# Performance work log

Hardware: AMD Instinct MI355X
Metric: run time of the kernel (lower is better)

## Reference

```python
import jax, jax.numpy as jnp
import numpy as np

N = 64          # truth table size (2^6)
NUM_VARS = 6
TOP_K = 16
BATCH = 524288
IN_DIM = 17 + TOP_K  # 33
HID = 64
OUT = 64
EPS_LN = 1e-5


def _hadamard(n: int) -> np.ndarray:
    H = np.array([[1.0]], dtype=np.float32)
    while H.shape[0] < n:
        H = np.block([[H, H], [H, -H]])
    return H

_HAMMING = np.array([bin(i).count('1') for i in range(N)], dtype=np.float32)


def _xavier(key, fan_in, fan_out):
    lim = np.sqrt(6.0 / (fan_in + fan_out)).astype(np.float32)
    return jax.random.uniform(key, (fan_in, fan_out), jnp.float32, -lim, lim)


def setup_inputs() -> dict:
    key = jax.random.key(0)
    ks = jax.random.split(key, 4)
    truth_table = jax.random.randint(ks[0], (BATCH, N), 0, 2).astype(jnp.int32)
    H = jnp.asarray(_hadamard(N))
    return {
        'truth_table': truth_table,
        'H': H,
        'W1': _xavier(ks[1], IN_DIM, HID), 'b1': jnp.zeros((HID,), jnp.float32),
        'g1': jnp.ones((HID,), jnp.float32), 'be1': jnp.zeros((HID,), jnp.float32),
        'W2': _xavier(ks[2], HID, HID), 'b2': jnp.zeros((HID,), jnp.float32),
        'g2': jnp.ones((HID,), jnp.float32), 'be2': jnp.zeros((HID,), jnp.float32),
        'W3': _xavier(ks[3], HID, OUT), 'b3': jnp.zeros((OUT,), jnp.float32),
    }


def _layernorm(x, g, b):
    m = jnp.mean(x, axis=-1, keepdims=True)
    v = jnp.mean((x - m) ** 2, axis=-1, keepdims=True)
    return (x - m) / jnp.sqrt(v + EPS_LN) * g + b


def _walsh_features(truth_table, H):
    # Walsh-Hadamard transform: torch.mm(H, f.T).T == f @ H.T == f @ H (H symmetric)
    f_polar = 1.0 - 2.0 * truth_table.astype(jnp.float32)  # [B, 64]
    walsh = f_polar @ H                                     # [B, 64]
    walsh_abs = jnp.abs(walsh)
    walsh_sq = walsh * walsh
    n = jnp.float32(N)

    # --- key coefficients (8d): W(0), W(2^i) i=0..5, W(n-1) ---
    key_idx = jnp.array([0, 1, 2, 4, 8, 16, 32, N - 1])
    key_coeffs = walsh[:, key_idx] / n                      # [B, 8]

    # --- spectral statistics (5d) ---
    threshold = 0.1 * n
    sparsity = jnp.mean((walsh_abs < threshold).astype(jnp.float32), axis=1, keepdims=True)
    max_abs = jnp.max(walsh_abs, axis=1, keepdims=True)
    max_mag = max_abs / n
    l1 = jnp.sum(walsh_abs, axis=1, keepdims=True) / (n * n)
    sumsq = jnp.sum(walsh_sq, axis=1, keepdims=True)
    l2 = jnp.sqrt(sumsq) / (n * n)
    p = walsh_sq / (sumsq + 1e-10)
    entropy = -jnp.sum(p * jnp.log(p + 1e-10), axis=1, keepdims=True) / jnp.log(n)
    spectral = jnp.concatenate([sparsity, max_mag, l1, l2, entropy], axis=1)  # [B, 5]

    # --- linearity indicators (4d) ---
    large_coeffs = jnp.sum((walsh_abs > 0.5 * n).astype(jnp.float32), axis=1, keepdims=True)
    is_linear = ((large_coeffs >= 1) & (large_coeffs <= 2)).astype(jnp.float32)
    nonlinearity = jnp.clip(0.5 - max_abs / (2 * n), 0.0, 0.5) * 2.0
    hw = jnp.asarray(_HAMMING)
    large_mask = (walsh_abs > threshold).astype(jnp.float32)
    degree = jnp.sum(large_mask * hw, axis=1, keepdims=True) / (
        jnp.sum(large_mask, axis=1, keepdims=True) + 1e-10) / NUM_VARS
    bent_mag = jnp.float32(2.0 ** (NUM_VARS / 2))  # 8.0
    bent_dev = jnp.mean(jnp.abs(walsh_abs - bent_mag) / bent_mag, axis=1, keepdims=True)
    is_bent = (bent_dev < 0.1).astype(jnp.float32)
    linearity = jnp.concatenate([is_linear, nonlinearity, degree, is_bent], axis=1)  # [B, 4]

    # --- top-k |W| coefficients (16d) ---
    topk = jax.lax.top_k(walsh_abs, TOP_K)[0] / n            # [B, 16]

    return jnp.concatenate([key_coeffs, spectral, linearity, topk], axis=1)  # [B, 33]


def reference(truth_table, H, W1, b1, g1, be1, W2, b2, g2, be2, W3, b3):
    feats = _walsh_features(truth_table, H)
    h = jax.nn.gelu(_layernorm(feats @ W1 + b1, g1, be1), approximate=False)
    # Dropout(0.1) is identity in eval mode
    h = jax.nn.gelu(_layernorm(h @ W2 + b2, g2, be2), approximate=False)
    return h @ W3 + b3  # [B, 64]
```

## Files before the change

kernel.cpp:

```cpp
#include <hip/hip_runtime.h>
#include <math.h>

#define TPB 256

typedef _Float16 half8 __attribute__((ext_vector_type(8)));
typedef _Float16 h2 __attribute__((ext_vector_type(2)));
typedef float f32x4 __attribute__((ext_vector_type(4)));

__device__ __forceinline__ int swz(int row, int col) {
    return row * 64 + ((((col >> 3) ^ row) & 7) << 3) + (col & 7);
}

__device__ __forceinline__ unsigned int pk_f16(float a, float b) {
    auto p = __builtin_amdgcn_cvt_pkrtz(a, b);
    return __builtin_bit_cast(unsigned int, p);
}

__device__ __forceinline__ float gelu_sig(float x) {
    float u = x * fmaf(0.0713548162f, x * x, 1.595769122f);
    float e = __expf(-u);
    return x * __builtin_amdgcn_rcpf(1.0f + e);
}

__device__ __forceinline__ void ce2(h2& x, h2& y) {
    h2 mx = __builtin_elementwise_max(x, y);
    h2 mn = __builtin_elementwise_min(x, y);
    x = mx; y = mn;
}

template<int CTRL>
__device__ __forceinline__ f32x4 dpp_add4(f32x4 x) {
#pragma unroll
    for (int r = 0; r < 4; ++r) {
        int o = __builtin_amdgcn_update_dpp(0, __float_as_int(x[r]),
                                            CTRL, 0xf, 0xf, false);
        x[r] += __int_as_float(o);
    }
    return x;
}
__device__ __forceinline__ f32x4 row_reduce16(f32x4 x) {
    x = dpp_add4<0x121>(x);
    x = dpp_add4<0x122>(x);
    x = dpp_add4<0x124>(x);
    x = dpp_add4<0x128>(x);
    return x;
}

__global__ void weight_stage_kernel(const float* __restrict__ W1,
                                    const float* __restrict__ W2,
                                    const float* __restrict__ W3,
                                    _Float16* __restrict__ wsW) {
    const int idx = blockIdx.x * 256 + threadIdx.x;
    if (idx >= 3 * 4 * 2 * 64 * 8) return;
    const int e    = idx & 7;
    const int lane = (idx >> 3) & 63;
    const int s    = (idx >> 9) & 1;
    const int nt   = (idx >> 10) & 3;
    const int L    = idx >> 12;
    const int g = lane >> 4, i = lane & 15;
    const int k = 32 * s + 8 * g + e;
    const int n = 4 * i + nt;
    const float* W = (L == 0) ? W1 : (L == 1) ? W2 : W3;
    const int K = (L == 0) ? 33 : 64;
    const float val = (k < K) ? W[k * 64 + n] : 0.0f;
    const _Float16 hi = (_Float16)val;
    const size_t base = ((((size_t)L * 4 + nt) * 2 + s) * 2) * 512
                        + (size_t)lane * 8 + e;
    wsW[base]       = hi;
    wsW[base + 512] = (_Float16)(val - (float)hi);
}

template<bool LAST>
__device__ __forceinline__ void mfma_layer(
    _Float16* actB,
    const _Float16* __restrict__ wsL,
    const float* bias, const float* gg, const float* bb,
    float* outp, int rowbase, int nrows)
{
    const int l = threadIdx.x & 63;
    const int g = l >> 4, i = l & 15;

    const half8* Bp = reinterpret_cast<const half8*>(wsL);
    half8 Bh[4][2], Bl[4][2];
#pragma unroll
    for (int nt = 0; nt < 4; ++nt) {
#pragma unroll
        for (int s = 0; s < 2; ++s) {
            Bh[nt][s] = Bp[((nt * 2 + s) * 2 + 0) * 64 + l];
            Bl[nt][s] = Bp[((nt * 2 + s) * 2 + 1) * 64 + l];
        }
    }
    const f32x4 bvv = *(const f32x4*)&bias[4 * i];
    f32x4 gvv, bevv;
    if (!LAST) {
        gvv  = *(const f32x4*)&gg[4 * i];
        bevv = *(const f32x4*)&bb[4 * i];
    }
    const bool full = LAST && (rowbase + 63 < nrows);

#pragma unroll
    for (int t = 0; t < 4; ++t) {
        const half8 A0 = *(const half8*)&actB[swz(16 * t + i, 8 * g)];
        const half8 A1 = *(const half8*)&actB[swz(16 * t + i, 32 + 8 * g)];
        f32x4 D[4];
#pragma unroll
        for (int nt = 0; nt < 4; ++nt) {
            f32x4 d = {bvv[nt], bvv[nt], bvv[nt], bvv[nt]};
            d = __builtin_amdgcn_mfma_f32_16x16x32_f16(A0, Bh[nt][0], d, 0, 0, 0);
            d = __builtin_amdgcn_mfma_f32_16x16x32_f16(A1, Bh[nt][1], d, 0, 0, 0);
            d = __builtin_amdgcn_mfma_f32_16x16x32_f16(A0, Bl[nt][0], d, 0, 0, 0);
            d = __builtin_amdgcn_mfma_f32_16x16x32_f16(A1, Bl[nt][1], d, 0, 0, 0);
            D[nt] = d;
        }
        if (LAST) {
#pragma unroll
            for (int r = 0; r < 4; ++r) {
                const int grow = rowbase + 16 * t + 4 * g + r;
                if (full || grow < nrows) {
                    f32x4 st = {D[0][r], D[1][r], D[2][r], D[3][r]};
                    *reinterpret_cast<f32x4*>(&outp[(size_t)grow * 64 + 4 * i]) = st;
                }
            }
        } else {
            f32x4 s4 = (D[0] + D[1]) + (D[2] + D[3]);
            f32x4 q4 = D[0] * D[0];
            q4 = D[1] * D[1] + q4;
            q4 = D[2] * D[2] + q4;
            q4 = D[3] * D[3] + q4;
            s4 = row_reduce16(s4);
            q4 = row_reduce16(q4);
            f32x4 mean = s4 * 0.015625f;
            f32x4 rstd;
#pragma unroll
            for (int r = 0; r < 4; ++r) {
                float var = q4[r] * 0.015625f - mean[r] * mean[r];
                rstd[r] = rsqrtf(var + 1e-5f);
            }
#pragma unroll
            for (int r = 0; r < 4; ++r) {
                float x0 = (D[0][r] - mean[r]) * rstd[r] * gvv[0] + bevv[0];
                float x1 = (D[1][r] - mean[r]) * rstd[r] * gvv[1] + bevv[1];
                float x2 = (D[2][r] - mean[r]) * rstd[r] * gvv[2] + bevv[2];
                float x3 = (D[3][r] - mean[r]) * rstd[r] * gvv[3] + bevv[3];
                uint2 st;
                st.x = pk_f16(gelu_sig(x0), gelu_sig(x1));
                st.y = pk_f16(gelu_sig(x2), gelu_sig(x3));
                *reinterpret_cast<uint2*>(
                    &actB[swz(16 * t + 4 * g + r, 4 * i)]) = st;
            }
        }
    }
    if (!LAST) asm volatile("s_waitcnt lgkmcnt(0)" ::: "memory");
}

__global__ __launch_bounds__(TPB, 2) void walsh_mlp_kernel(
    const int* __restrict__ tt,
    const float* __restrict__ b1,
    const float* __restrict__ g1, const float* __restrict__ be1,
    const float* __restrict__ b2,
    const float* __restrict__ g2, const float* __restrict__ be2,
    const float* __restrict__ b3,
    const _Float16* __restrict__ wsW,
    float* __restrict__ out, int nrows)
{
    __shared__ __align__(16) _Float16 sAct[4][64][64];
    __shared__ float sP[7 * 64];
    __shared__ float entLUT[33];

    const int tid = threadIdx.x;
    if (tid < 64) {
        sP[tid]       = g1[tid];
        sP[64 + tid]  = be1[tid];
        sP[128 + tid] = g2[tid];
        sP[192 + tid] = be2[tid];
        sP[256 + tid] = b1[tid];
        sP[320 + tid] = b2[tid];
        sP[384 + tid] = b3[tid];
    }
    if (tid < 33) {
        const float a = 2.0f * (float)tid;
        const float p = (a * a) * 2.44140625e-4f;
        entLUT[tid] = -(p * __logf(p + 1e-10f));
    }
    __syncthreads();

    const int row = blockIdx.x * TPB + tid;
    const int rowc = (row < nrows) ? row : (nrows - 1);

    float v[64];
    const int4* t4 = reinterpret_cast<const int4*>(tt + (size_t)rowc * 64);
#pragma unroll
    for (int q = 0; q < 16; ++q) {
        int4 a = t4[q];
        v[4 * q + 0] = 1.0f - 2.0f * (float)a.x;
        v[4 * q + 1] = 1.0f - 2.0f * (float)a.y;
        v[4 * q + 2] = 1.0f - 2.0f * (float)a.z;
        v[4 * q + 3] = 1.0f - 2.0f * (float)a.w;
    }

#pragma unroll
    for (int h = 1; h < 64; h <<= 1) {
#pragma unroll
        for (int i = 0; i < 64; ++i) {
            if ((i & h) == 0) {
                float a = v[i], b = v[i | h];
                v[i] = a + b;
                v[i | h] = a - b;
            }
        }
    }

    const float inv_n = 1.0f / 64.0f;
    float f[17];
    f[0] = v[0] * inv_n;  f[1] = v[1] * inv_n;  f[2] = v[2] * inv_n;
    f[3] = v[4] * inv_n;  f[4] = v[8] * inv_n;  f[5] = v[16] * inv_n;
    f[6] = v[32] * inv_n; f[7] = v[63] * inv_n;

    float sumabs = 0.f, maxab = 0.f, cnt_sp = 0.f, cnt_lg = 0.f;
    float sum_hw = 0.f, bent = 0.f, ent = 0.f;
#pragma unroll
    for (int i = 0; i < 64; ++i) {
        float a = fabsf(v[i]);
        v[i] = a;
        sumabs += a;
        maxab = fmaxf(maxab, a);
        cnt_sp += (a < 6.4f) ? 1.0f : 0.0f;
        sum_hw += (a < 6.4f) ? 0.0f : (float)__popc(i);
        cnt_lg += (a > 32.0f) ? 1.0f : 0.0f;
        bent += fabsf(a - 8.0f);
        ent += entLUT[((int)a) >> 1];
    }

    f[8]  = cnt_sp * inv_n;
    f[9]  = maxab * inv_n;
    f[10] = sumabs * (1.0f / 4096.0f);
    f[11] = 0.015625f;
    f[12] = ent * 0.24044917348149316f;
    f[13] = (cnt_lg >= 0.5f && cnt_lg <= 2.5f) ? 1.0f : 0.0f;
    f[14] = fmaxf(0.0f, 0.5f - maxab * (1.0f / 128.0f)) * 2.0f;
    f[15] = sum_hw / (64.0f - cnt_sp + 1e-10f) * (1.0f / 6.0f);
    f[16] = (bent < 51.2f) ? 1.0f : 0.0f;

    h2 t2[16];
    {
        h2 hv[32];
#pragma unroll
        for (int i = 0; i < 32; ++i)
            hv[i] = __builtin_bit_cast(h2, pk_f16(v[i], v[i + 32]));

#pragma unroll
        for (int base = 0; base < 32; base += 16) {
#pragma unroll
            for (int p = 1; p < 16; p <<= 1) {
#pragma unroll
                for (int k = p; k >= 1; k >>= 1) {
#pragma unroll
                    for (int j = k & (p - 1); j + k < 16; j += 2 * k) {
#pragma unroll
                        for (int i = 0; i < k; ++i) {
                            if (i + j + k < 16 &&
                                (i + j) / (2 * p) == (i + j + k) / (2 * p))
                                ce2(hv[base + i + j], hv[base + i + j + k]);
                        }
                    }
                }
            }
        }
        h2 mm[16];
#pragma unroll
        for (int i = 0; i < 16; ++i)
            mm[i] = __builtin_elementwise_max(hv[i], hv[31 - i]);
#pragma unroll
        for (int d = 8; d >= 1; d >>= 1) {
#pragma unroll
            for (int i = 0; i < 16; ++i)
                if ((i & d) == 0) ce2(mm[i], mm[i + d]);
        }
#pragma unroll
        for (int i = 0; i < 16; ++i) {
            unsigned m = __builtin_bit_cast(unsigned, mm[15 - i]);
            unsigned sw = __builtin_amdgcn_alignbit(m, m, 16);
            t2[i] = __builtin_elementwise_max(mm[i], __builtin_bit_cast(h2, sw));
        }
#pragma unroll
        for (int d = 8; d >= 1; d >>= 1) {
#pragma unroll
            for (int i = 0; i < 16; ++i)
                if ((i & d) == 0) ce2(t2[i], t2[i + d]);
        }
        const h2 hs = {(_Float16)0.015625f, (_Float16)0.015625f};
#pragma unroll
        for (int i = 0; i < 16; ++i) t2[i] = t2[i] * hs;
    }

    const int w = tid >> 6, l = tid & 63;
    _Float16* actB = &sAct[w][0][0];

    {
        unsigned wd[32];
#pragma unroll
        for (int j = 0; j < 8; ++j) wd[j] = pk_f16(f[2 * j], f[2 * j + 1]);
        {
            unsigned lo = (unsigned)__builtin_bit_cast(unsigned short,
                                                       (_Float16)f[16]);
            wd[8] = lo | (__builtin_bit_cast(unsigned, t2[0]) << 16);
        }
#pragma unroll
        for (int m = 0; m < 7; ++m)
            wd[9 + m] = (__builtin_bit_cast(unsigned, t2[2 * m + 1]) & 0xFFFFu)
                      | (__builtin_bit_cast(unsigned, t2[2 * m + 2]) << 16);
        wd[16] = __builtin_bit_cast(unsigned, t2[15]) & 0xFFFFu;
#pragma unroll
        for (int j = 17; j < 32; ++j) wd[j] = 0u;
#pragma unroll
        for (int c = 0; c < 8; ++c) {
            uint4 st;
            st.x = wd[4 * c + 0]; st.y = wd[4 * c + 1];
            st.z = wd[4 * c + 2]; st.w = wd[4 * c + 3];
            *reinterpret_cast<uint4*>(&actB[swz(l, c * 8)]) = st;
        }
    }
    asm volatile("s_waitcnt lgkmcnt(0)" ::: "memory");

    const int rowbase = blockIdx.x * TPB + w * 64;
    mfma_layer<false>(actB, wsW,         sP + 256, sP + 0,   sP + 64,
                      nullptr, 0, 0);
    mfma_layer<false>(actB, wsW + 8192,  sP + 320, sP + 128, sP + 192,
                      nullptr, 0, 0);
    mfma_layer<true >(actB, wsW + 16384, sP + 384, nullptr,  nullptr,
                      out, rowbase, nrows);
}

extern "C" void kernel_launch(void* const* d_in, const int* in_sizes, int n_in,
                              void* d_out, int out_size, void* d_ws, size_t ws_size,
                              hipStream_t stream) {
    const int*   tt  = (const int*)d_in[0];
    const float* W1  = (const float*)d_in[2];
    const float* b1  = (const float*)d_in[3];
    const float* g1  = (const float*)d_in[4];
    const float* be1 = (const float*)d_in[5];
    const float* W2  = (const float*)d_in[6];
    const float* b2  = (const float*)d_in[7];
    const float* g2  = (const float*)d_in[8];
    const float* be2 = (const float*)d_in[9];
    const float* W3  = (const float*)d_in[10];
    const float* b3  = (const float*)d_in[11];
    float* out = (float*)d_out;
    _Float16* wsW = (_Float16*)d_ws;

    const int nrows = in_sizes[0] / 64;

    hipLaunchKernelGGL(weight_stage_kernel, dim3(48), dim3(256), 0, stream,
                       W1, W2, W3, wsW);

    const int grid = (nrows + TPB - 1) / TPB;
    hipLaunchKernelGGL(walsh_mlp_kernel, dim3(grid), dim3(TPB), 0, stream,
                       tt, b1, g1, be1, b2, g2, be2, b3, wsW, out, nrows);
}
```

Before: 92.08 us.

## Run Walsh transform and spectral statistics in packed fp16, shrink block size

Replaces the fp32 64-point butterfly with a packed-half 32-lane butterfly. Each packed lane holds entries i and i+32, built by bit-manipulating the truth table bits into ±1 halves, and the last stage is done on extraction. The spectral reductions (sum, max, bent deviation, sparsity and large counts, hamming-weight sum) move to packed fp16 arithmetic with clamp-based indicator tricks. This halves VALU work and register pressure. The block size also drops from 256 to 192 with matching shared memory. fp16 accumulation of sums up to 4096 loses precision and could shift the features slightly.

```diff
diff --git a/kernel.cpp b/kernel.cpp
--- a/kernel.cpp
+++ b/kernel.cpp
@@ -1,7 +1,7 @@
 #include <hip/hip_runtime.h>
 #include <math.h>
 
-#define TPB 256
+#define TPB 192
 
 typedef _Float16 half8 __attribute__((ext_vector_type(8)));
 typedef _Float16 h2 __attribute__((ext_vector_type(2)));
@@ -163,7 +163,7 @@
     const _Float16* __restrict__ wsW,
     float* __restrict__ out, int nrows)
 {
-    __shared__ __align__(16) _Float16 sAct[4][64][64];
+    __shared__ __align__(16) _Float16 sAct[3][64][64];
     __shared__ float sP[7 * 64];
     __shared__ float entLUT[33];
 
@@ -187,49 +187,82 @@
     const int row = blockIdx.x * TPB + tid;
     const int rowc = (row < nrows) ? row : (nrows - 1);
 
-    float v[64];
+    h2 p[32];
     const int4* t4 = reinterpret_cast<const int4*>(tt + (size_t)rowc * 64);
 #pragma unroll
-    for (int q = 0; q < 16; ++q) {
-        int4 a = t4[q];
-        v[4 * q + 0] = 1.0f - 2.0f * (float)a.x;
-        v[4 * q + 1] = 1.0f - 2.0f * (float)a.y;
-        v[4 * q + 2] = 1.0f - 2.0f * (float)a.z;
-        v[4 * q + 3] = 1.0f - 2.0f * (float)a.w;
-    }
-
-#pragma unroll
-    for (int h = 1; h < 64; h <<= 1) {
-#pragma unroll
-        for (int i = 0; i < 64; ++i) {
+    for (int q = 0; q < 8; ++q) {
+        int4 alo = t4[q];
+        int4 ahi = t4[q + 8];
+        p[4 * q + 0] = __builtin_bit_cast(h2,
+            0x3C003C00u | ((unsigned)alo.x << 15) | ((unsigned)ahi.x << 31));
+        p[4 * q + 1] = __builtin_bit_cast(h2,
+            0x3C003C00u | ((unsigned)alo.y << 15) | ((unsigned)ahi.y << 31));
+        p[4 * q + 2] = __builtin_bit_cast(h2,
+            0x3C003C00u | ((unsigned)alo.z << 15) | ((unsigned)ahi.z << 31));
+        p[4 * q + 3] = __builtin_bit_cast(h2,
+            0x3C003C00u | ((unsigned)alo.w << 15) | ((unsigned)ahi.w << 31));
+    }
+
+#pragma unroll
+    for (int h = 1; h < 32; h <<= 1) {
+#pragma unroll
+        for (int i = 0; i < 32; ++i) {
             if ((i & h) == 0) {
-                float a = v[i], b = v[i | h];
-                v[i] = a + b;
-                v[i | h] = a - b;
+                h2 a = p[i], b = p[i | h];
+                p[i] = a + b;
+                p[i | h] = a - b;
             }
         }
     }
 
     const float inv_n = 1.0f / 64.0f;
     float f[17];
-    f[0] = v[0] * inv_n;  f[1] = v[1] * inv_n;  f[2] = v[2] * inv_n;
-    f[3] = v[4] * inv_n;  f[4] = v[8] * inv_n;  f[5] = v[16] * inv_n;
-    f[6] = v[32] * inv_n; f[7] = v[63] * inv_n;
-
-    float sumabs = 0.f, maxab = 0.f, cnt_sp = 0.f, cnt_lg = 0.f;
-    float sum_hw = 0.f, bent = 0.f, ent = 0.f;
-#pragma unroll
-    for (int i = 0; i < 64; ++i) {
-        float a = fabsf(v[i]);
-        v[i] = a;
-        sumabs += a;
-        maxab = fmaxf(maxab, a);
-        cnt_sp += (a < 6.4f) ? 1.0f : 0.0f;
-        sum_hw += (a < 6.4f) ? 0.0f : (float)__popc(i);
-        cnt_lg += (a > 32.0f) ? 1.0f : 0.0f;
-        bent += fabsf(a - 8.0f);
-        ent += entLUT[((int)a) >> 1];
-    }
+    h2 habs[32];
+    const h2 kONE  = {(_Float16)1.0f, (_Float16)1.0f};
+    const h2 kZERO = {(_Float16)0.0f, (_Float16)0.0f};
+    const h2 k64   = {(_Float16)64.0f, (_Float16)64.0f};
+    const h2 kCsp  = {(_Float16)409.5f, (_Float16)409.5f};
+    const h2 kClg  = {(_Float16)-2080.0f, (_Float16)-2080.0f};
+    const h2 kM8   = {(_Float16)-8.0f, (_Float16)-8.0f};
+    h2 sum2 = kZERO, max2 = kZERO, bent2 = kZERO;
+    h2 csp2 = kZERO, clg2 = kZERO, chw2 = kZERO;
+    float ent = 0.0f;
+#pragma unroll
+    for (int i = 0; i < 32; ++i) {
+        const float lo = (float)p[i][0], hi = (float)p[i][1];
+        const float a0 = lo + hi;
+        const float a1 = lo - hi;
+        if (i == 0)  { f[0] = a0 * inv_n; f[6] = a1 * inv_n; }
+        if (i == 1)  f[1] = a0 * inv_n;
+        if (i == 2)  f[2] = a0 * inv_n;
+        if (i == 4)  f[3] = a0 * inv_n;
+        if (i == 8)  f[4] = a0 * inv_n;
+        if (i == 16) f[5] = a0 * inv_n;
+        if (i == 31) f[7] = a1 * inv_n;
+        const h2 a = __builtin_bit_cast(h2, pk_f16(a0, a1) & 0x7FFF7FFFu);
+        habs[i] = a;
+        sum2 = sum2 + a;
+        max2 = __builtin_elementwise_max(max2, a);
+        bent2 = bent2 + __builtin_bit_cast(h2,
+            __builtin_bit_cast(unsigned, a + kM8) & 0x7FFF7FFFu);
+        const h2 ssp = __builtin_elementwise_min(kONE,
+            __builtin_elementwise_max(kZERO, kCsp - a * k64));
+        csp2 = csp2 + ssp;
+        clg2 = clg2 + __builtin_elementwise_min(kONE,
+            __builtin_elementwise_max(kZERO, a * k64 + kClg));
+        const float PC = (float)__builtin_popcount(i);
+        const h2 hp = {(_Float16)PC, (_Float16)PC};
+        chw2 = chw2 + (kONE - ssp) * hp;
+        ent += entLUT[((int)fabsf(a0)) >> 1];
+        ent += entLUT[((int)fabsf(a1)) >> 1];
+    }
+    const float sumabs = (float)sum2[0] + (float)sum2[1];
+    const float maxab  = fmaxf((float)max2[0], (float)max2[1]);
+    const float bent   = (float)bent2[0] + (float)bent2[1];
+    const float cnt_sp = (float)csp2[0] + (float)csp2[1];
+    const float cnt_lg = (float)clg2[0] + (float)clg2[1];
+    const float sum_hw = (float)chw2[0] + (float)chw2[1]
+                       + (32.0f - (float)csp2[1]);
 
     f[8]  = cnt_sp * inv_n;
     f[9]  = maxab * inv_n;
@@ -243,24 +276,19 @@
 
     h2 t2[16];
     {
-        h2 hv[32];
-#pragma unroll
-        for (int i = 0; i < 32; ++i)
-            hv[i] = __builtin_bit_cast(h2, pk_f16(v[i], v[i + 32]));
-
 #pragma unroll
         for (int base = 0; base < 32; base += 16) {
 #pragma unroll
-            for (int p = 1; p < 16; p <<= 1) {
-#pragma unroll
-                for (int k = p; k >= 1; k >>= 1) {
-#pragma unroll
-                    for (int j = k & (p - 1); j + k < 16; j += 2 * k) {
+            for (int pp = 1; pp < 16; pp <<= 1) {
+#pragma unroll
+                for (int k = pp; k >= 1; k >>= 1) {
+#pragma unroll
+                    for (int j = k & (pp - 1); j + k < 16; j += 2 * k) {
 #pragma unroll
                         for (int i = 0; i < k; ++i) {
                             if (i + j + k < 16 &&
-                                (i + j) / (2 * p) == (i + j + k) / (2 * p))
-                                ce2(hv[base + i + j], hv[base + i + j + k]);
+                                (i + j) / (2 * pp) == (i + j + k) / (2 * pp))
+                                ce2(habs[base + i + j], habs[base + i + j + k]);
                         }
                     }
                 }
@@ -269,7 +297,7 @@
         h2 mm[16];
 #pragma unroll
         for (int i = 0; i < 16; ++i)
-            mm[i] = __builtin_elementwise_max(hv[i], hv[31 - i]);
+            mm[i] = __builtin_elementwise_max(habs[i], habs[31 - i]);
 #pragma unroll
         for (int d = 8; d >= 1; d >>= 1) {
 #pragma unroll
```

After: 97.69 us. 6.1% more time.
